# Optimization experiments

Measured on AMD Instinct MI355X. Metric: run time of the kernel, lower is better.

The kernel has to match this reference:

```python
import jax, jax.numpy as jnp
import numpy as np

WS = 8          # window size
HEADS = 16      # num heads

def conv2d(x, w, padding=0, groups=1):
    return jax.lax.conv_general_dilated(
        x, w, window_strides=(1, 1),
        padding=((padding, padding), (padding, padding)),
        feature_group_count=groups,
        dimension_numbers=('NCHW', 'OIHW', 'NCHW'))

def bn(x, scale, bias):  # inference BN folded into per-channel affine
    return x * scale[None, :, None, None] + bias[None, :, None, None]

def relative_position_index(ws):
    coords = np.stack(np.meshgrid(np.arange(ws), np.arange(ws), indexing='ij'))  # (2, ws, ws)
    cf = coords.reshape(2, -1)
    rc = (cf[:, :, None] - cf[:, None, :]).transpose(1, 2, 0)  # (n, n, 2)
    rc[:, :, 0] += ws - 1
    rc[:, :, 1] += ws - 1
    rc[:, :, 0] *= 2 * ws - 1
    return rc.sum(-1)  # (n, n) int

def avg_pool(x, kh, kw, ph, pw):
    # AvgPool2d with count_include_pad=True (zero pad, divide by full kernel size)
    s = jax.lax.reduce_window(x, 0.0, jax.lax.add, (1, 1, kh, kw), (1, 1, 1, 1),
                              ((0, 0), (0, 0), (ph, ph), (pw, pw)))
    return s / (kh * kw)

def setup_inputs() -> dict:
    key = jax.random.key(0)
    ks = jax.random.split(key, 12)
    C = 256
    x = jax.random.normal(ks[0], (4, C, 128, 128), dtype=jnp.float32)
    inp = {
        'x': x,
        'qkv_w':     jax.random.normal(ks[1], (3 * C, C, 1, 1), jnp.float32) * 0.05,
        'local1_w':  jax.random.normal(ks[2], (C, C, 3, 3), jnp.float32) * 0.05,
        'local1_scale': jnp.ones((C,), jnp.float32),
        'local1_bias':  jnp.zeros((C,), jnp.float32),
        'local2_w':  jax.random.normal(ks[3], (C, C, 1, 1), jnp.float32) * 0.05,
        'local2_scale': jnp.ones((C,), jnp.float32),
        'local2_bias':  jnp.zeros((C,), jnp.float32),
        'dw_w':      jax.random.normal(ks[4], (C, 1, WS, WS), jnp.float32) * 0.05,
        'proj_scale': jnp.ones((C,), jnp.float32),
        'proj_bias':  jnp.zeros((C,), jnp.float32),
        'pw_w':      jax.random.normal(ks[5], (C, C, 1, 1), jnp.float32) * 0.05,
        'rel_bias_table': jax.random.normal(ks[6], ((2 * WS - 1) ** 2, HEADS), jnp.float32) * 0.02,
    }
    return inp

def reference(x, qkv_w, local1_w, local1_scale, local1_bias,
              local2_w, local2_scale, local2_bias,
              dw_w, proj_scale, proj_bias, pw_w, rel_bias_table):
    B, C, H, W = x.shape
    ws, h = WS, HEADS
    d = C // h
    scale = d ** -0.5

    # local branches
    local = bn(conv2d(x, local2_w, padding=0), local2_scale, local2_bias) \
          + bn(conv2d(x, local1_w, padding=1), local1_scale, local1_bias)

    # reflect-pad to multiple of ws (static shapes)
    pad_h = (ws - H % ws) % ws
    pad_w = (ws - W % ws) % ws
    xp = x
    if pad_w:
        xp = jnp.pad(xp, ((0, 0), (0, 0), (0, 0), (0, pad_w)), mode='reflect')
    if pad_h:
        xp = jnp.pad(xp, ((0, 0), (0, 0), (0, pad_h), (0, 0)), mode='reflect')
    Hp, Wp = xp.shape[2], xp.shape[3]
    hh, ww = Hp // ws, Wp // ws

    # qkv: 1x1 conv, then window partition
    qkv = conv2d(xp, qkv_w)  # (B, 3C, Hp, Wp)
    qkv = qkv.reshape(B, 3, h, d, hh, ws, ww, ws)
    qkv = qkv.transpose(1, 0, 4, 6, 2, 5, 7, 3)  # (3, B, hh, ww, h, ws, ws, d)
    qkv = qkv.reshape(3, B * hh * ww, h, ws * ws, d)
    q, k, v = qkv[0], qkv[1], qkv[2]

    dots = jnp.einsum('whid,whjd->whij', q, k) * scale
    rpi = relative_position_index(ws)  # (n, n)
    bias = rel_bias_table[rpi.reshape(-1)].reshape(ws * ws, ws * ws, h)
    dots = dots + bias.transpose(2, 0, 1)[None]
    attn = jax.nn.softmax(dots, axis=-1)
    out = jnp.einsum('whij,whjd->whid', attn, v)

    # windows back to image
    out = out.reshape(B, hh, ww, h, ws, ws, d)
    out = out.transpose(0, 3, 6, 1, 4, 2, 5).reshape(B, C, Hp, Wp)
    out = out[:, :, :H, :W]

    # boundary smoothing avg pools (reflect pad 1 then zero-padded avg pool)
    ax = avg_pool(jnp.pad(out, ((0, 0), (0, 0), (0, 1), (0, 0)), mode='reflect'),
                  ws, 1, ws // 2 - 1, 0)
    ay = avg_pool(jnp.pad(out, ((0, 0), (0, 0), (0, 0), (0, 1)), mode='reflect'),
                  1, ws, 0, ws // 2 - 1)
    out = ax + ay + local

    # pad_out + separable conv projection
    out = jnp.pad(out, ((0, 0), (0, 0), (0, 1), (0, 1)), mode='reflect')
    out = conv2d(out, dw_w, padding=(ws - 1) // 2, groups=C)  # depthwise 8x8
    out = bn(out, proj_scale, proj_bias)
    out = conv2d(out, pw_w)  # pointwise 1x1
    return out[:, :, :H, :W]
```

## Files before the change

### kernel.cpp

```cpp
#include <hip/hip_runtime.h>
#include <cstddef>

#define HH 128
#define WW2 128
#define HWSZ (HH*WW2)
#define CCH 256

typedef __attribute__((ext_vector_type(8))) short short8v;
typedef __attribute__((ext_vector_type(16))) float f32x16;
typedef __attribute__((ext_vector_type(4)))  float f32x4;

__device__ __forceinline__ ushort bf16rte(float v) {
    uint u = __float_as_uint(v);
    uint r = u + 0x7FFFu + ((u >> 16) & 1u);
    return (ushort)(r >> 16);
}

__global__ __launch_bounds__(256) void k_fold(const float* __restrict__ l1w, const float* __restrict__ l1s,
                                              const float* __restrict__ l1b, const float* __restrict__ l2w,
                                              const float* __restrict__ l2s, const float* __restrict__ l2b,
                                              float* __restrict__ Wf, float* __restrict__ biasf) {
    int idx = blockIdx.x * 256 + threadIdx.x;
    if (idx < 2304 * 256) {
        int co = idx & 255;
        int i2 = idx >> 8;
        int ci = i2 / 9;
        int k  = i2 - ci * 9;
        float w = l1s[co] * l1w[co * 2304 + ci * 9 + k];
        if (k == 4) w += l2s[co] * l2w[co * 256 + ci];
        Wf[i2 * 256 + co] = w;
    }
    if (idx < 256) biasf[idx] = l1b[idx] + l2b[idx];
}

__global__ __launch_bounds__(256) void k_wsplit(const float* __restrict__ Wf,
                                                ushort* __restrict__ ahi, ushort* __restrict__ alo) {
    int idx = blockIdx.x * 256 + threadIdx.x;
    if (idx >= 589824) return;
    int j    = idx & 7;
    int lane = (idx >> 3) & 63;
    int t2   = idx >> 9;
    int kb   = t2 % 144;
    int cob  = t2 / 144;
    int cc  = kb / 18; int rem = kb - cc * 18; int tap = rem >> 1; int ks = rem & 1;
    int ci  = cc * 32 + ks * 16 + ((lane >> 5) << 3) + j;
    int co  = cob * 32 + (lane & 31);
    float v = Wf[(size_t)(ci * 9 + tap) * 256 + co];
    ushort h = bf16rte(v);
    float hf = __uint_as_float((uint)h << 16);
    ushort l = bf16rte(v - hf);
    ahi[idx] = h;
    alo[idx] = l;
}

__global__ __launch_bounds__(256) void k_aswz(const float* __restrict__ qkvw,
                                              ushort* __restrict__ aqh, ushort* __restrict__ aql) {
    int idx = blockIdx.x * 256 + threadIdx.x;
    if (idx >= 196608) return;
    int j    = idx & 7;
    int lane = (idx >> 3) & 63;
    int t2   = idx >> 9;
    int kk   = t2 & 7;
    int hp   = t2 >> 3;
    int p    = hp % 3, h = hp / 3;
    int co = p * 256 + h * 16 + (lane & 15);
    int ci = kk * 32 + ((lane >> 4) << 3) + j;
    float v = qkvw[(size_t)co * 256 + ci];
    ushort hi = bf16rte(v);
    float hf = __uint_as_float((uint)hi << 16);
    aqh[idx] = hi;
    aql[idx] = bf16rte(v - hf);
}

__global__ __launch_bounds__(256) void k_pswz(const float* __restrict__ pww,
                                              ushort* __restrict__ apwh, ushort* __restrict__ apwl) {
    int idx = blockIdx.x * 256 + threadIdx.x;
    if (idx >= 65536) return;
    int j    = idx & 7;
    int lane = (idx >> 3) & 63;
    int t2   = idx >> 9;
    int ks   = t2 & 15;
    int cob  = t2 >> 4;
    int co = cob * 32 + (lane & 31);
    int ci = ks * 16 + ((lane >> 5) << 3) + j;
    float v = pww[(size_t)co * 256 + ci];
    ushort h = bf16rte(v);
    float hf = __uint_as_float((uint)h << 16);
    apwh[idx] = h;
    apwl[idx] = bf16rte(v - hf);
}

__global__ __launch_bounds__(256) void k_cvt(const float* __restrict__ x,
                                             ushort* __restrict__ xhi, ushort* __restrict__ xlo) {
    __shared__ uint pk[32 * 265];
    int t = threadIdx.x;
    int bid = blockIdx.x;
    int b = bid >> 9;
    int px0 = (bid & 511) * 32;
    const float* xb = x + (size_t)b * CCH * HWSZ;
    for (int step = 0; step < 32; ++step) {
        int ci = step * 8 + (t >> 5);
        float v = xb[(size_t)ci * HWSZ + px0 + (t & 31)];
        ushort h = bf16rte(v);
        float hf = __uint_as_float((uint)h << 16);
        ushort l = bf16rte(v - hf);
        pk[(t & 31) * 265 + ci] = ((uint)h << 16) | l;
    }
    __syncthreads();
    int pxl = t >> 3, o = t & 7;
    uint* hp = (uint*)xhi;
    uint* lp = (uint*)xlo;
    size_t pb2 = ((size_t)b * HWSZ + px0 + pxl) * 128;
#pragma unroll
    for (int m = 0; m < 16; ++m) {
        int cip = m * 16 + o * 2;
        uint p0 = pk[pxl * 265 + cip];
        uint p1 = pk[pxl * 265 + cip + 1];
        hp[pb2 + m * 8 + o] = (p1 & 0xFFFF0000u) | (p0 >> 16);
        lp[pb2 + m * 8 + o] = (p1 << 16) | (p0 & 0xFFFFu);
    }
}

__global__ __launch_bounds__(256) void k_conv3m(const ushort* __restrict__ xhi, const ushort* __restrict__ xlo,
                                                const ushort* __restrict__ afr_hi, const ushort* __restrict__ afr_lo,
                                                const float* __restrict__ biasf, float* __restrict__ outp) {
    __shared__ __align__(16) ushort Xsh[12960];
    char* xsb = (char*)Xsh;

    int t = threadIdx.x;
    int bid = blockIdx.x;
    int cb = bid & 1;
    int t2 = bid >> 1;
    int tile_c = t2 & 7;
    int tile_r = (t2 >> 3) & 15;
    int b = t2 >> 7;
    int x0 = tile_c * 16, y0 = tile_r * 8;

    int w = t >> 6, lane = t & 63;
    int co_w = cb * 128 + (w >> 1) * 64;
    int pr0 = (w & 1) * 4;
    int pr_l = (lane & 31) >> 4;
    int pc = lane & 15;
    int kl = lane >> 5;
    int lb0 = (pr0 + 0 + pr_l) * 1296 + pc * 72 + kl * 16;
    int lb1 = (pr0 + 2 + pr_l) * 1296 + pc * 72 + kl * 16;

    const short8v* Ahi = (const short8v*)afr_hi;
    const short8v* Alo = (const short8v*)afr_lo;
    int cobase = (co_w >> 5) * 144 * 64;

    f32x16 c00 = {}, c01 = {}, c10 = {}, c11 = {};

    for (int cc = 0; cc < 8; ++cc) {
        __syncthreads();
#pragma unroll
        for (int it = 0; it < 6; ++it) {
            int i = t + it * 256;
            if (i < 1440) {
                int oct = i & 3;
                int j2 = i >> 2;
                int plane = j2 & 1;
                int loc = j2 >> 1;
                int r = loc / 18, c = loc - r * 18;
                int gy = y0 - 1 + r, gx = x0 - 1 + c;
                uint4 v = make_uint4(0u, 0u, 0u, 0u);
                if (gy >= 0 && gy < 128 && gx >= 0 && gx < 128) {
                    const ushort* src = plane ? xlo : xhi;
                    v = *(const uint4*)(src + ((size_t)(b * HWSZ + gy * 128 + gx) * 256 + cc * 32 + oct * 8));
                }
                *(uint4*)(xsb + plane * 12960 + loc * 72 + oct * 16) = v;
            }
        }
        __syncthreads();

        int baseA = cobase + cc * 18 * 64 + lane;
#pragma unroll
        for (int tap = 0; tap < 9; ++tap) {
            const int ky = tap / 3, kx = tap - ky * 3;
#pragma unroll
            for (int ks = 0; ks < 2; ++ks) {
                const int boff = ky * 1296 + kx * 72 + ks * 32;
                short8v b0h = *(const short8v*)(xsb + lb0 + boff);
                short8v b0l = *(const short8v*)(xsb + lb0 + boff + 12960);
                short8v b1h = *(const short8v*)(xsb + lb1 + boff);
                short8v b1l = *(const short8v*)(xsb + lb1 + boff + 12960);
                int ai = baseA + (tap * 2 + ks) * 64;
                short8v a0h = Ahi[ai];
                short8v a0l = Alo[ai];
                short8v a1h = Ahi[ai + 144 * 64];
                short8v a1l = Alo[ai + 144 * 64];
                c00 = __builtin_amdgcn_mfma_f32_32x32x16_bf16(a0h, b0h, c00, 0, 0, 0);
                c00 = __builtin_amdgcn_mfma_f32_32x32x16_bf16(a0h, b0l, c00, 0, 0, 0);
                c00 = __builtin_amdgcn_mfma_f32_32x32x16_bf16(a0l, b0h, c00, 0, 0, 0);
                c01 = __builtin_amdgcn_mfma_f32_32x32x16_bf16(a0h, b1h, c01, 0, 0, 0);
                c01 = __builtin_amdgcn_mfma_f32_32x32x16_bf16(a0h, b1l, c01, 0, 0, 0);
                c01 = __builtin_amdgcn_mfma_f32_32x32x16_bf16(a0l, b1h, c01, 0, 0, 0);
                c10 = __builtin_amdgcn_mfma_f32_32x32x16_bf16(a1h, b0h, c10, 0, 0, 0);
                c10 = __builtin_amdgcn_mfma_f32_32x32x16_bf16(a1h, b0l, c10, 0, 0, 0);
                c10 = __builtin_amdgcn_mfma_f32_32x32x16_bf16(a1l, b0h, c10, 0, 0, 0);
                c11 = __builtin_amdgcn_mfma_f32_32x32x16_bf16(a1h, b1h, c11, 0, 0, 0);
                c11 = __builtin_amdgcn_mfma_f32_32x32x16_bf16(a1h, b1l, c11, 0, 0, 0);
                c11 = __builtin_amdgcn_mfma_f32_32x32x16_bf16(a1l, b1h, c11, 0, 0, 0);
            }
        }
    }

    int colg = x0 + pc;
    int row0 = y0 + pr0 + pr_l;
    int row1 = row0 + 2;
#pragma unroll
    for (int r = 0; r < 16; ++r) {
        int rr = (r & 3) + 8 * (r >> 2) + 4 * kl;
        {
            int co = co_w + rr;
            float bv = biasf[co];
            float* ob = outp + ((size_t)(b * CCH + co)) * HWSZ;
            ob[row0 * 128 + colg] = c00[r] + bv;
            ob[row1 * 128 + colg] = c01[r] + bv;
        }
        {
            int co = co_w + 32 + rr;
            float bv = biasf[co];
            float* ob = outp + ((size_t)(b * CCH + co)) * HWSZ;
            ob[row0 * 128 + colg] = c10[r] + bv;
            ob[row1 * 128 + colg] = c11[r] + bv;
        }
    }
}

__global__ __launch_bounds__(256, 3) void k_attn(const ushort* __restrict__ xhi, const ushort* __restrict__ xlo,
                                                 const ushort* __restrict__ aqh, const ushort* __restrict__ aql,
                                                 const float* __restrict__ bt, float* __restrict__ attnout) {
    __shared__ float qkvb[2][48 * 64];
    __shared__ float btl[16 * 225];

    int t = threadIdx.x;
    int wv = __builtin_amdgcn_readfirstlane(t >> 6);
    int lane = t & 63;
    int widx = blockIdx.x;
    int b = widx >> 8;
    int rem = widx & 255;
    int hy = rem >> 4, wx = rem & 15;
    int y0 = hy * 8, x0 = wx * 8;

    for (int i = t; i < 3600; i += 256) {
        int rpi = i >> 4, hh = i & 15;
        btl[hh * 225 + rpi] = bt[i];
    }

    int tokb = (wv << 4) | (lane & 15);
    int pixb = (y0 + (tokb >> 3)) * 128 + (x0 + (tokb & 7));
    const ushort* xbh = xhi + ((size_t)b * HWSZ + pixb) * 256 + ((lane >> 4) << 3);
    const ushort* xbl = xlo + ((size_t)b * HWSZ + pixb) * 256 + ((lane >> 4) << 3);
    short8v bh_[8], bl_[8];
#pragma unroll
    for (int kk = 0; kk < 8; ++kk) {
        bh_[kk] = *(const short8v*)(xbh + kk * 32);
        bl_[kk] = *(const short8v*)(xbl + kk * 32);
    }

    const short8v* AhB = (const short8v*)aqh + lane;
    const short8v* AlB = (const short8v*)aql + lane;
    int wrow = ((lane >> 4) << 2);
    int wtok = (wv << 4) + (lane & 15);

    {
#pragma unroll
        for (int p = 0; p < 3; ++p) {
            f32x4 c = {};
#pragma unroll
            for (int kk = 0; kk < 8; ++kk) {
                short8v ah = AhB[(p * 8 + kk) * 64];
                short8v al = AlB[(p * 8 + kk) * 64];
                c = __builtin_amdgcn_mfma_f32_16x16x32_bf16(ah, bh_[kk], c, 0, 0, 0);
                c = __builtin_amdgcn_mfma_f32_16x16x32_bf16(ah, bl_[kk], c, 0, 0, 0);
                c = __builtin_amdgcn_mfma_f32_16x16x32_bf16(al, bh_[kk], c, 0, 0, 0);
            }
            float* bw = &qkvb[0][(p * 16 + wrow) * 64 + wtok];
            bw[0] = c[0]; bw[64] = c[1]; bw[128] = c[2]; bw[192] = c[3];
        }
    }
    __syncthreads();

    int irow = wv * 16 + (lane & 15);
    int jg = lane >> 4;
    int iy = irow >> 3, ix = irow & 7;

#pragma unroll 2
    for (int h = 0; h < 16; ++h) {
        int h2 = (h + 1) & 15;
        int nb = (h + 1) & 1;
        const short8v* Ah = AhB + (size_t)h2 * 24 * 64;
        const short8v* Al = AlB + (size_t)h2 * 24 * 64;
#pragma unroll
        for (int p = 0; p < 3; ++p) {
            f32x4 c = {};
#pragma unroll
            for (int kk = 0; kk < 8; ++kk) {
                short8v ah = Ah[(p * 8 + kk) * 64];
                short8v al = Al[(p * 8 + kk) * 64];
                c = __builtin_amdgcn_mfma_f32_16x16x32_bf16(ah, bh_[kk], c, 0, 0, 0);
                c = __builtin_amdgcn_mfma_f32_16x16x32_bf16(ah, bl_[kk], c, 0, 0, 0);
                c = __builtin_amdgcn_mfma_f32_16x16x32_bf16(al, bh_[kk], c, 0, 0, 0);
            }
            float* bw = &qkvb[nb][(p * 16 + wrow) * 64 + wtok];
            bw[0] = c[0]; bw[64] = c[1]; bw[128] = c[2]; bw[192] = c[3];
        }

        const float* buf = qkvb[h & 1];
        float qd[16];
#pragma unroll
        for (int d = 0; d < 16; ++d) qd[d] = buf[d * 64 + irow];
        float s[16];
#pragma unroll
        for (int jj = 0; jj < 16; ++jj) s[jj] = 0.f;
#pragma unroll
        for (int d = 0; d < 16; ++d) {
            const float* kp = &buf[(16 + d) * 64 + jg * 16];
#pragma unroll
            for (int m = 0; m < 4; ++m) {
                float4 kv = *(const float4*)(kp + m * 4);
                s[m * 4 + 0] += qd[d] * kv.x;
                s[m * 4 + 1] += qd[d] * kv.y;
                s[m * 4 + 2] += qd[d] * kv.z;
                s[m * 4 + 3] += qd[d] * kv.w;
            }
        }
#pragma unroll
        for (int jj = 0; jj < 16; ++jj) {
            int j = jg * 16 + jj;
            int jy = j >> 3, jx = j & 7;
            int rpi = (iy - jy + 7) * 15 + (ix - jx + 7);
            s[jj] = s[jj] * 0.25f + btl[h * 225 + rpi];
        }
        float mx = s[0];
#pragma unroll
        for (int jj = 1; jj < 16; ++jj) mx = fmaxf(mx, s[jj]);
        mx = fmaxf(mx, __shfl_xor(mx, 16));
        mx = fmaxf(mx, __shfl_xor(mx, 32));
        float ls = 0.f;
#pragma unroll
        for (int jj = 0; jj < 16; ++jj) { s[jj] = __expf(s[jj] - mx); ls += s[jj]; }
        ls += __shfl_xor(ls, 16);
        ls += __shfl_xor(ls, 32);
        float inv = 1.0f / ls;
#pragma unroll
        for (int d = 0; d < 16; ++d) {
            const float* vp = &buf[(32 + d) * 64 + jg * 16];
            float o0 = 0.f, o1 = 0.f;
#pragma unroll
            for (int m = 0; m < 4; ++m) {
                float4 vvv = *(const float4*)(vp + m * 4);
                o0 += s[m * 4 + 0] * vvv.x + s[m * 4 + 1] * vvv.y;
                o1 += s[m * 4 + 2] * vvv.z + s[m * 4 + 3] * vvv.w;
            }
            float o = o0 + o1;
            o += __shfl_xor(o, 16);
            o += __shfl_xor(o, 32);
            if (jg == 0)
                attnout[((size_t)(b * CCH + h * 16 + d)) * HWSZ + (y0 + iy) * 128 + (x0 + ix)] = o * inv;
        }
        __syncthreads();
    }
}

__global__ __launch_bounds__(256) void k_pools(const float* __restrict__ attnout, const float* __restrict__ localb,
                                               float* __restrict__ sbuf) {
    for (int i = blockIdx.x * 256 + threadIdx.x; i < 4 * CCH * HWSZ; i += gridDim.x * 256) {
        int xc = i & 127;
        int y  = (i >> 7) & 127;
        int bc = i >> 14;
        const float* pl = attnout + (size_t)bc * HWSZ;
        float axs = 0.f;
#pragma unroll
        for (int d = -3; d <= 4; ++d) {
            int t2 = y + d;
            if (t2 >= 0 && t2 < 128) axs += pl[t2 * 128 + xc];
        }
        if (y >= 124) axs += pl[126 * 128 + xc];
        float ays = 0.f;
#pragma unroll
        for (int d = -3; d <= 4; ++d) {
            int t2 = xc + d;
            if (t2 >= 0 && t2 < 128) ays += pl[y * 128 + t2];
        }
        if (xc >= 124) ays += pl[y * 128 + 126];
        sbuf[i] = (axs + ays) * 0.125f + localb[i];
    }
}

__device__ __forceinline__ void dw_loadrow(const float* __restrict__ sp, int trow, int j, float* dst) {
    if (trow < 0 || trow > 128) {
#pragma unroll
        for (int q = 0; q < 8; ++q) dst[q] = 0.f;
        return;
    }
    int sr = (trow == 128) ? 126 : trow;
    const float* rp = sp + sr * 128;
#pragma unroll
    for (int q = 0; q < 8; ++q) {
        int col = j - 3 + q;
        float v = 0.f;
        if (col >= 0 && col <= 128) v = rp[(col == 128) ? 126 : col];
        dst[q] = v;
    }
}

__global__ __launch_bounds__(256) void k_dw(const float* __restrict__ sbuf, const float* __restrict__ dww,
                                            const float* __restrict__ pscale, const float* __restrict__ pbias,
                                            float* __restrict__ tbuf) {
    int t = threadIdx.x;
    int j = t & 127;
    int half = __builtin_amdgcn_readfirstlane(t >> 7);
    int bid = blockIdx.x;
    int c = (bid & 127) * 2 + half;
    int b = bid >> 7;
    const float* sp = sbuf + ((size_t)(b * CCH + c)) * HWSZ;
    float wloc[64];
    const float* dwp = dww + c * 64;
#pragma unroll
    for (int i = 0; i < 64; ++i) wloc[i] = dwp[i];
    float scale = pscale[c], bias = pbias[c];

    float rbuf[8][8];
#pragma unroll
    for (int tr = -3; tr <= 4; ++tr) {
        dw_loadrow(sp, tr, j, rbuf[(tr + 8) & 7]);
    }
    float* op = tbuf + ((size_t)(b * CCH + c)) * HWSZ;
    for (int yb = 0; yb < 16; ++yb) {
#pragma unroll
        for (int k = 0; k < 8; ++k) {
            int y = yb * 8 + k;
            float a0 = 0.f, a1 = 0.f, a2 = 0.f, a3 = 0.f;
#pragma unroll
            for (int p = 0; p < 8; ++p) {
                const int slot = (k + 5 + p) & 7;
                float part = 0.f;
#pragma unroll
                for (int q = 0; q < 8; ++q) part += wloc[p * 8 + q] * rbuf[slot][q];
                if ((p & 3) == 0) a0 += part;
                else if ((p & 3) == 1) a1 += part;
                else if ((p & 3) == 2) a2 += part;
                else a3 += part;
            }
            op[y * 128 + j] = scale * ((a0 + a1) + (a2 + a3)) + bias;
            dw_loadrow(sp, y + 5, j, rbuf[(k + 5) & 7]);
        }
    }
}

__global__ __launch_bounds__(256) void k_pwm(const float* __restrict__ tbuf,
                                             const ushort* __restrict__ apwh, const ushort* __restrict__ apwl,
                                             float* __restrict__ outp) {
    __shared__ __align__(16) ushort pBh[32][264];
    __shared__ __align__(16) ushort pBl[32][264];

    int t = threadIdx.x;
    int bid = blockIdx.x;
    int b = bid >> 9;
    int px0 = (bid & 511) * 32;
    int px = t & 31;

    for (int it = 0; it < 32; ++it) {
        int ci = it * 8 + (t >> 5);
        float v = tbuf[((size_t)(b * CCH + ci)) * HWSZ + px0 + px];
        ushort h = bf16rte(v);
        float hf = __uint_as_float((uint)h << 16);
        pBh[px][ci] = h;
        pBl[px][ci] = bf16rte(v - hf);
    }
    __syncthreads();

    int w = t >> 6, lane = t & 63;
    int kl = lane >> 5;
    int pc = lane & 31;
    const short8v* Ah = (const short8v*)apwh;
    const short8v* Al = (const short8v*)apwl;
    int a0base = ((w * 2) * 16) * 64 + lane;
    int a1base = ((w * 2 + 1) * 16) * 64 + lane;

    f32x16 c0 = {}, c1 = {};
#pragma unroll
    for (int ks = 0; ks < 16; ++ks) {
        short8v bh = *(const short8v*)&pBh[pc][ks * 16 + kl * 8];
        short8v bl = *(const short8v*)&pBl[pc][ks * 16 + kl * 8];
        short8v a0h = Ah[a0base + ks * 64];
        short8v a0l = Al[a0base + ks * 64];
        short8v a1h = Ah[a1base + ks * 64];
        short8v a1l = Al[a1base + ks * 64];
        c0 = __builtin_amdgcn_mfma_f32_32x32x16_bf16(a0h, bh, c0, 0, 0, 0);
        c0 = __builtin_amdgcn_mfma_f32_32x32x16_bf16(a0h, bl, c0, 0, 0, 0);
        c0 = __builtin_amdgcn_mfma_f32_32x32x16_bf16(a0l, bh, c0, 0, 0, 0);
        c1 = __builtin_amdgcn_mfma_f32_32x32x16_bf16(a1h, bh, c1, 0, 0, 0);
        c1 = __builtin_amdgcn_mfma_f32_32x32x16_bf16(a1h, bl, c1, 0, 0, 0);
        c1 = __builtin_amdgcn_mfma_f32_32x32x16_bf16(a1l, bh, c1, 0, 0, 0);
    }

#pragma unroll
    for (int r = 0; r < 16; ++r) {
        int rr = (r & 3) + 8 * (r >> 2) + 4 * kl;
        {
            int co = w * 64 + rr;
            outp[((size_t)(b * CCH + co)) * HWSZ + px0 + pc] = c0[r];
        }
        {
            int co = w * 64 + 32 + rr;
            outp[((size_t)(b * CCH + co)) * HWSZ + px0 + pc] = c1[r];
        }
    }
}

extern "C" void kernel_launch(void* const* d_in, const int* in_sizes, int n_in,
                              void* d_out, int out_size, void* d_ws, size_t ws_size,
                              hipStream_t stream) {
    const float* x    = (const float*)d_in[0];
    const float* qkvw = (const float*)d_in[1];
    const float* l1w  = (const float*)d_in[2];
    const float* l1s  = (const float*)d_in[3];
    const float* l1b  = (const float*)d_in[4];
    const float* l2w  = (const float*)d_in[5];
    const float* l2s  = (const float*)d_in[6];
    const float* l2b  = (const float*)d_in[7];
    const float* dww  = (const float*)d_in[8];
    const float* ps   = (const float*)d_in[9];
    const float* pb   = (const float*)d_in[10];
    const float* pww  = (const float*)d_in[11];
    const float* bt   = (const float*)d_in[12];
    float* out = (float*)d_out;
    float* wsf = (float*)d_ws;

    const size_t nWf = 589824;
    const size_t nPlane = 16777216;
    const size_t nAq = 196608;
    const size_t nApw = 65536;
    size_t need = (nWf + 256 + 3 * nPlane) * sizeof(float)
                + (2 * 589824 + 2 * nAq + 2 * nApw) * sizeof(ushort);
    if (ws_size < need) return;

    float* Wf      = wsf;
    float* biasf   = wsf + nWf;
    float* attnout = wsf + nWf + 256;
    float* localb  = attnout + nPlane;
    float* sbuf    = localb + nPlane;
    float* tbuf    = attnout;
    ushort* xhi = (ushort*)sbuf;
    ushort* xlo = xhi + nPlane;
    ushort* ahi = (ushort*)(sbuf + nPlane);
    ushort* alo = ahi + 589824;
    ushort* aqh = alo + 589824;
    ushort* aql = aqh + nAq;
    ushort* apwh = aql + nAq;
    ushort* apwl = apwh + nApw;

    k_fold  <<<2304, 256, 0, stream>>>(l1w, l1s, l1b, l2w, l2s, l2b, Wf, biasf);
    k_wsplit<<<2304, 256, 0, stream>>>(Wf, ahi, alo);
    k_aswz  <<<768,  256, 0, stream>>>(qkvw, aqh, aql);
    k_pswz  <<<256,  256, 0, stream>>>(pww, apwh, apwl);
    k_cvt   <<<2048, 256, 0, stream>>>(x, xhi, xlo);
    k_conv3m<<<1024, 256, 0, stream>>>(xhi, xlo, ahi, alo, biasf, localb);
    k_attn  <<<1024, 256, 0, stream>>>(xhi, xlo, aqh, aql, bt, attnout);
    k_pools <<<4096, 256, 0, stream>>>(attnout, localb, sbuf);
    k_dw    <<<512,  256, 0, stream>>>(sbuf, dww, ps, pb, tbuf);
    k_pwm   <<<2048, 256, 0, stream>>>(tbuf, apwh, apwl, out);
}
```

Measured before the change: 796.5 us.

## Double-buffer conv3x3 input tile in LDS with register prefetch

The 3x3 conv kernel now keeps two LDS buffers for the input halo tile. It loads the next channel chunk from global memory into registers before running the MFMA loop on the current buffer, then writes those registers to the other buffer after a barrier. The aim is to hide global load latency behind the MFMA work and to drop one barrier per iteration. In exchange it doubles LDS use to about 52KB, which may lower occupancy, and adds 24 VGPRs for staging.

```diff
diff --git a/kernel.cpp b/kernel.cpp
--- a/kernel.cpp
+++ b/kernel.cpp
@@ -124,7 +124,7 @@
 __global__ __launch_bounds__(256) void k_conv3m(const ushort* __restrict__ xhi, const ushort* __restrict__ xlo,
                                                 const ushort* __restrict__ afr_hi, const ushort* __restrict__ afr_lo,
                                                 const float* __restrict__ biasf, float* __restrict__ outp) {
-    __shared__ __align__(16) ushort Xsh[12960];
+    __shared__ __align__(16) ushort Xsh[2 * 12960];
     char* xsb = (char*)Xsh;
 
     int t = threadIdx.x;
@@ -151,8 +151,28 @@
 
     f32x16 c00 = {}, c01 = {}, c10 = {}, c11 = {};
 
-    for (int cc = 0; cc < 8; ++cc) {
-        __syncthreads();
+    uint4 st[6];
+    auto stage_issue = [&](int cc) {
+#pragma unroll
+        for (int it = 0; it < 6; ++it) {
+            int i = t + it * 256;
+            uint4 v = make_uint4(0u, 0u, 0u, 0u);
+            if (i < 1440) {
+                int oct = i & 3;
+                int j2 = i >> 2;
+                int plane = j2 & 1;
+                int loc = j2 >> 1;
+                int r = loc / 18, c = loc - r * 18;
+                int gy = y0 - 1 + r, gx = x0 - 1 + c;
+                if (gy >= 0 && gy < 128 && gx >= 0 && gx < 128) {
+                    const ushort* src = plane ? xlo : xhi;
+                    v = *(const uint4*)(src + ((size_t)(b * HWSZ + gy * 128 + gx) * 256 + cc * 32 + oct * 8));
+                }
+            }
+            st[it] = v;
+        }
+    };
+    auto stage_write = [&](int buf) {
 #pragma unroll
         for (int it = 0; it < 6; ++it) {
             int i = t + it * 256;
@@ -161,17 +181,20 @@
                 int j2 = i >> 2;
                 int plane = j2 & 1;
                 int loc = j2 >> 1;
-                int r = loc / 18, c = loc - r * 18;
-                int gy = y0 - 1 + r, gx = x0 - 1 + c;
-                uint4 v = make_uint4(0u, 0u, 0u, 0u);
-                if (gy >= 0 && gy < 128 && gx >= 0 && gx < 128) {
-                    const ushort* src = plane ? xlo : xhi;
-                    v = *(const uint4*)(src + ((size_t)(b * HWSZ + gy * 128 + gx) * 256 + cc * 32 + oct * 8));
-                }
-                *(uint4*)(xsb + plane * 12960 + loc * 72 + oct * 16) = v;
-            }
-        }
-        __syncthreads();
+                *(uint4*)(xsb + buf * 25920 + plane * 12960 + loc * 72 + oct * 16) = st[it];
+            }
+        }
+    };
+
+    stage_issue(0);
+    asm volatile("s_waitcnt vmcnt(0)" ::: "memory");
+    stage_write(0);
+    asm volatile("s_waitcnt lgkmcnt(0)" ::: "memory");
+    __builtin_amdgcn_s_barrier();
+
+    for (int cc = 0; cc < 8; ++cc) {
+        if (cc < 7) stage_issue(cc + 1);
+        int bufoff = (cc & 1) * 25920;
 
         int baseA = cobase + cc * 18 * 64 + lane;
 #pragma unroll
@@ -179,7 +202,7 @@
             const int ky = tap / 3, kx = tap - ky * 3;
 #pragma unroll
             for (int ks = 0; ks < 2; ++ks) {
-                const int boff = ky * 1296 + kx * 72 + ks * 32;
+                const int boff = bufoff + ky * 1296 + kx * 72 + ks * 32;
                 short8v b0h = *(const short8v*)(xsb + lb0 + boff);
                 short8v b0l = *(const short8v*)(xsb + lb0 + boff + 12960);
                 short8v b1h = *(const short8v*)(xsb + lb1 + boff);
@@ -203,6 +226,13 @@
                 c11 = __builtin_amdgcn_mfma_f32_32x32x16_bf16(a1l, b1h, c11, 0, 0, 0);
             }
         }
+
+        if (cc < 7) {
+            asm volatile("s_waitcnt vmcnt(0)" ::: "memory");
+            stage_write((cc + 1) & 1);
+            asm volatile("s_waitcnt lgkmcnt(0)" ::: "memory");
+            __builtin_amdgcn_s_barrier();
+        }
     }
 
     int colg = x0 + pc;
```

After: 794.0 us. No clear change (-0.3%).

## Merge local 3x3 conv and window attention into one interleaved kernel

Applied to the files above, without the earlier changes.

Folds the conv3m and attention kernels into a single launch where even blocks run the 3x3 conv tile and odd blocks run a window's attention, sharing one LDS allocation. The aim is to run the MFMA-heavy conv alongside the more ALU/LDS-bound attention on the same CUs and to drop a launch boundary and its tail. In exchange, both block types now take the larger shared-memory footprint and the register budget of the heavier path. Attention also loses its launch_bounds occupancy hint, which may reduce its occupancy.

```diff
diff --git a/kernel.cpp b/kernel.cpp
--- a/kernel.cpp
+++ b/kernel.cpp
@@ -121,246 +121,245 @@
     }
 }
 
-__global__ __launch_bounds__(256) void k_conv3m(const ushort* __restrict__ xhi, const ushort* __restrict__ xlo,
-                                                const ushort* __restrict__ afr_hi, const ushort* __restrict__ afr_lo,
-                                                const float* __restrict__ biasf, float* __restrict__ outp) {
-    __shared__ __align__(16) ushort Xsh[12960];
-    char* xsb = (char*)Xsh;
-
+__global__ __launch_bounds__(256) void k_convattn(const ushort* __restrict__ xhi, const ushort* __restrict__ xlo,
+                                                  const ushort* __restrict__ afr_hi, const ushort* __restrict__ afr_lo,
+                                                  const ushort* __restrict__ aqh, const ushort* __restrict__ aql,
+                                                  const float* __restrict__ biasf, const float* __restrict__ bt,
+                                                  float* __restrict__ localb, float* __restrict__ attnout) {
+    __shared__ __align__(16) char smem[38976];
     int t = threadIdx.x;
-    int bid = blockIdx.x;
-    int cb = bid & 1;
-    int t2 = bid >> 1;
-    int tile_c = t2 & 7;
-    int tile_r = (t2 >> 3) & 15;
-    int b = t2 >> 7;
-    int x0 = tile_c * 16, y0 = tile_r * 8;
-
-    int w = t >> 6, lane = t & 63;
-    int co_w = cb * 128 + (w >> 1) * 64;
-    int pr0 = (w & 1) * 4;
-    int pr_l = (lane & 31) >> 4;
-    int pc = lane & 15;
-    int kl = lane >> 5;
-    int lb0 = (pr0 + 0 + pr_l) * 1296 + pc * 72 + kl * 16;
-    int lb1 = (pr0 + 2 + pr_l) * 1296 + pc * 72 + kl * 16;
-
-    const short8v* Ahi = (const short8v*)afr_hi;
-    const short8v* Alo = (const short8v*)afr_lo;
-    int cobase = (co_w >> 5) * 144 * 64;
-
-    f32x16 c00 = {}, c01 = {}, c10 = {}, c11 = {};
-
-    for (int cc = 0; cc < 8; ++cc) {
+
+    if ((blockIdx.x & 1) == 0) {
+        char* xsb = smem;
+        int bid = blockIdx.x >> 1;
+        int cb = bid & 1;
+        int t2 = bid >> 1;
+        int tile_c = t2 & 7;
+        int tile_r = (t2 >> 3) & 15;
+        int b = t2 >> 7;
+        int x0 = tile_c * 16, y0 = tile_r * 8;
+
+        int w = t >> 6, lane = t & 63;
+        int co_w = cb * 128 + (w >> 1) * 64;
+        int pr0 = (w & 1) * 4;
+        int pr_l = (lane & 31) >> 4;
+        int pc = lane & 15;
+        int kl = lane >> 5;
+        int lb0 = (pr0 + 0 + pr_l) * 1296 + pc * 72 + kl * 16;
+        int lb1 = (pr0 + 2 + pr_l) * 1296 + pc * 72 + kl * 16;
+
+        const short8v* Ahi = (const short8v*)afr_hi;
+        const short8v* Alo = (const short8v*)afr_lo;
+        int cobase = (co_w >> 5) * 144 * 64;
+
+        f32x16 c00 = {}, c01 = {}, c10 = {}, c11 = {};
+
+        for (int cc = 0; cc < 8; ++cc) {
+            __syncthreads();
+#pragma unroll
+            for (int it = 0; it < 6; ++it) {
+                int i = t + it * 256;
+                if (i < 1440) {
+                    int oct = i & 3;
+                    int j2 = i >> 2;
+                    int plane = j2 & 1;
+                    int loc = j2 >> 1;
+                    int r = loc / 18, c = loc - r * 18;
+                    int gy = y0 - 1 + r, gx = x0 - 1 + c;
+                    uint4 v = make_uint4(0u, 0u, 0u, 0u);
+                    if (gy >= 0 && gy < 128 && gx >= 0 && gx < 128) {
+                        const ushort* src = plane ? xlo : xhi;
+                        v = *(const uint4*)(src + ((size_t)(b * HWSZ + gy * 128 + gx) * 256 + cc * 32 + oct * 8));
+                    }
+                    *(uint4*)(xsb + plane * 12960 + loc * 72 + oct * 16) = v;
+                }
+            }
+            __syncthreads();
+
+            int baseA = cobase + cc * 18 * 64 + lane;
+#pragma unroll
+            for (int tap = 0; tap < 9; ++tap) {
+                const int ky = tap / 3, kx = tap - ky * 3;
+#pragma unroll
+                for (int ks = 0; ks < 2; ++ks) {
+                    const int boff = ky * 1296 + kx * 72 + ks * 32;
+                    short8v b0h = *(const short8v*)(xsb + lb0 + boff);
+                    short8v b0l = *(const short8v*)(xsb + lb0 + boff + 12960);
+                    short8v b1h = *(const short8v*)(xsb + lb1 + boff);
+                    short8v b1l = *(const short8v*)(xsb + lb1 + boff + 12960);
+                    int ai = baseA + (tap * 2 + ks) * 64;
+                    short8v a0h = Ahi[ai];
+                    short8v a0l = Alo[ai];
+                    short8v a1h = Ahi[ai + 144 * 64];
+                    short8v a1l = Alo[ai + 144 * 64];
+                    c00 = __builtin_amdgcn_mfma_f32_32x32x16_bf16(a0h, b0h, c00, 0, 0, 0);
+                    c00 = __builtin_amdgcn_mfma_f32_32x32x16_bf16(a0h, b0l, c00, 0, 0, 0);
+                    c00 = __builtin_amdgcn_mfma_f32_32x32x16_bf16(a0l, b0h, c00, 0, 0, 0);
+                    c01 = __builtin_amdgcn_mfma_f32_32x32x16_bf16(a0h, b1h, c01, 0, 0, 0);
+                    c01 = __builtin_amdgcn_mfma_f32_32x32x16_bf16(a0h, b1l, c01, 0, 0, 0);
+                    c01 = __builtin_amdgcn_mfma_f32_32x32x16_bf16(a0l, b1h, c01, 0, 0, 0);
+                    c10 = __builtin_amdgcn_mfma_f32_32x32x16_bf16(a1h, b0h, c10, 0, 0, 0);
+                    c10 = __builtin_amdgcn_mfma_f32_32x32x16_bf16(a1h, b0l, c10, 0, 0, 0);
+                    c10 = __builtin_amdgcn_mfma_f32_32x32x16_bf16(a1l, b0h, c10, 0, 0, 0);
+                    c11 = __builtin_amdgcn_mfma_f32_32x32x16_bf16(a1h, b1h, c11, 0, 0, 0);
+                    c11 = __builtin_amdgcn_mfma_f32_32x32x16_bf16(a1h, b1l, c11, 0, 0, 0);
+                    c11 = __builtin_amdgcn_mfma_f32_32x32x16_bf16(a1l, b1h, c11, 0, 0, 0);
+                }
+            }
+        }
+
+        int colg = x0 + pc;
+        int row0 = y0 + pr0 + pr_l;
+        int row1 = row0 + 2;
+#pragma unroll
+        for (int r = 0; r < 16; ++r) {
+            int rr = (r & 3) + 8 * (r >> 2) + 4 * kl;
+            {
+                int co = co_w + rr;
+                float bv = biasf[co];
+                float* ob = localb + ((size_t)(b * CCH + co)) * HWSZ;
+                ob[row0 * 128 + colg] = c00[r] + bv;
+                ob[row1 * 128 + colg] = c01[r] + bv;
+            }
+            {
+                int co = co_w + 32 + rr;
+                float bv = biasf[co];
+                float* ob = localb + ((size_t)(b * CCH + co)) * HWSZ;
+                ob[row0 * 128 + colg] = c10[r] + bv;
+                ob[row1 * 128 + colg] = c11[r] + bv;
+            }
+        }
+    } else {
+        float* qkvb = (float*)smem;
+        float* btl  = (float*)(smem + 24576);
+
+        int wv = __builtin_amdgcn_readfirstlane(t >> 6);
+        int lane = t & 63;
+        int widx = blockIdx.x >> 1;
+        int b = widx >> 8;
+        int rem = widx & 255;
+        int hy = rem >> 4, wx = rem & 15;
+        int y0 = hy * 8, x0 = wx * 8;
+
+        for (int i = t; i < 3600; i += 256) {
+            int rpi = i >> 4, hh = i & 15;
+            btl[hh * 225 + rpi] = bt[i];
+        }
+
+        int tokb = (wv << 4) | (lane & 15);
+        int pixb = (y0 + (tokb >> 3)) * 128 + (x0 + (tokb & 7));
+        const ushort* xbh = xhi + ((size_t)b * HWSZ + pixb) * 256 + ((lane >> 4) << 3);
+        const ushort* xbl = xlo + ((size_t)b * HWSZ + pixb) * 256 + ((lane >> 4) << 3);
+        short8v bh_[8], bl_[8];
+#pragma unroll
+        for (int kk = 0; kk < 8; ++kk) {
+            bh_[kk] = *(const short8v*)(xbh + kk * 32);
+            bl_[kk] = *(const short8v*)(xbl + kk * 32);
+        }
+
+        const short8v* AhB = (const short8v*)aqh + lane;
+        const short8v* AlB = (const short8v*)aql + lane;
+        int wrow = ((lane >> 4) << 2);
+        int wtok = (wv << 4) + (lane & 15);
+
+        {
+#pragma unroll
+            for (int p = 0; p < 3; ++p) {
+                f32x4 c = {};
+#pragma unroll
+                for (int kk = 0; kk < 8; ++kk) {
+                    short8v ah = AhB[(p * 8 + kk) * 64];
+                    short8v al = AlB[(p * 8 + kk) * 64];
+                    c = __builtin_amdgcn_mfma_f32_16x16x32_bf16(ah, bh_[kk], c, 0, 0, 0);
+                    c = __builtin_amdgcn_mfma_f32_16x16x32_bf16(ah, bl_[kk], c, 0, 0, 0);
+                    c = __builtin_amdgcn_mfma_f32_16x16x32_bf16(al, bh_[kk], c, 0, 0, 0);
+                }
+                float* bw = &qkvb[(p * 16 + wrow) * 64 + wtok];
+                bw[0] = c[0]; bw[64] = c[1]; bw[128] = c[2]; bw[192] = c[3];
+            }
+        }
         __syncthreads();
-#pragma unroll
-        for (int it = 0; it < 6; ++it) {
-            int i = t + it * 256;
-            if (i < 1440) {
-                int oct = i & 3;
-                int j2 = i >> 2;
-                int plane = j2 & 1;
-                int loc = j2 >> 1;
-                int r = loc / 18, c = loc - r * 18;
-                int gy = y0 - 1 + r, gx = x0 - 1 + c;
-                uint4 v = make_uint4(0u, 0u, 0u, 0u);
-                if (gy >= 0 && gy < 128 && gx >= 0 && gx < 128) {
-                    const ushort* src = plane ? xlo : xhi;
-                    v = *(const uint4*)(src + ((size_t)(b * HWSZ + gy * 128 + gx) * 256 + cc * 32 + oct * 8));
+
+        int irow = wv * 16 + (lane & 15);
+        int jg = lane >> 4;
+        int iy = irow >> 3, ix = irow & 7;
+
+#pragma unroll 2
+        for (int h = 0; h < 16; ++h) {
+            int h2 = (h + 1) & 15;
+            int nb = (h + 1) & 1;
+            const short8v* Ah = AhB + (size_t)h2 * 24 * 64;
+            const short8v* Al = AlB + (size_t)h2 * 24 * 64;
+#pragma unroll
+            for (int p = 0; p < 3; ++p) {
+                f32x4 c = {};
+#pragma unroll
+                for (int kk = 0; kk < 8; ++kk) {
+                    short8v ah = Ah[(p * 8 + kk) * 64];
+                    short8v al = Al[(p * 8 + kk) * 64];
+                    c = __builtin_amdgcn_mfma_f32_16x16x32_bf16(ah, bh_[kk], c, 0, 0, 0);
+                    c = __builtin_amdgcn_mfma_f32_16x16x32_bf16(ah, bl_[kk], c, 0, 0, 0);
+                    c = __builtin_amdgcn_mfma_f32_16x16x32_bf16(al, bh_[kk], c, 0, 0, 0);
                 }
-                *(uint4*)(xsb + plane * 12960 + loc * 72 + oct * 16) = v;
-            }
-        }
-        __syncthreads();
-
-        int baseA = cobase + cc * 18 * 64 + lane;
-#pragma unroll
-        for (int tap = 0; tap < 9; ++tap) {
-            const int ky = tap / 3, kx = tap - ky * 3;
-#pragma unroll
-            for (int ks = 0; ks < 2; ++ks) {
-                const int boff = ky * 1296 + kx * 72 + ks * 32;
-                short8v b0h = *(const short8v*)(xsb + lb0 + boff);
-                short8v b0l = *(const short8v*)(xsb + lb0 + boff + 12960);
-                short8v b1h = *(const short8v*)(xsb + lb1 + boff);
-                short8v b1l = *(const short8v*)(xsb + lb1 + boff + 12960);
-                int ai = baseA + (tap * 2 + ks) * 64;
-                short8v a0h = Ahi[ai];
-                short8v a0l = Alo[ai];
-                short8v a1h = Ahi[ai + 144 * 64];
-                short8v a1l = Alo[ai + 144 * 64];
-                c00 = __builtin_amdgcn_mfma_f32_32x32x16_bf16(a0h, b0h, c00, 0, 0, 0);
-                c00 = __builtin_amdgcn_mfma_f32_32x32x16_bf16(a0h, b0l, c00, 0, 0, 0);
-                c00 = __builtin_amdgcn_mfma_f32_32x32x16_bf16(a0l, b0h, c00, 0, 0, 0);
-                c01 = __builtin_amdgcn_mfma_f32_32x32x16_bf16(a0h, b1h, c01, 0, 0, 0);
-                c01 = __builtin_amdgcn_mfma_f32_32x32x16_bf16(a0h, b1l, c01, 0, 0, 0);
-                c01 = __builtin_amdgcn_mfma_f32_32x32x16_bf16(a0l, b1h, c01, 0, 0, 0);
-                c10 = __builtin_amdgcn_mfma_f32_32x32x16_bf16(a1h, b0h, c10, 0, 0, 0);
-                c10 = __builtin_amdgcn_mfma_f32_32x32x16_bf16(a1h, b0l, c10, 0, 0, 0);
-                c10 = __builtin_amdgcn_mfma_f32_32x32x16_bf16(a1l, b0h, c10, 0, 0, 0);
-                c11 = __builtin_amdgcn_mfma_f32_32x32x16_bf16(a1h, b1h, c11, 0, 0, 0);
-                c11 = __builtin_amdgcn_mfma_f32_32x32x16_bf16(a1h, b1l, c11, 0, 0, 0);
-                c11 = __builtin_amdgcn_mfma_f32_32x32x16_bf16(a1l, b1h, c11, 0, 0, 0);
-            }
-        }
-    }
-
-    int colg = x0 + pc;
-    int row0 = y0 + pr0 + pr_l;
-    int row1 = row0 + 2;
-#pragma unroll
-    for (int r = 0; r < 16; ++r) {
-        int rr = (r & 3) + 8 * (r >> 2) + 4 * kl;
-        {
-            int co = co_w + rr;
-            float bv = biasf[co];
-            float* ob = outp + ((size_t)(b * CCH + co)) * HWSZ;
-            ob[row0 * 128 + colg] = c00[r] + bv;
-            ob[row1 * 128 + colg] = c01[r] + bv;
-        }
-        {
-            int co = co_w + 32 + rr;
-            float bv = biasf[co];
-            float* ob = outp + ((size_t)(b * CCH + co)) * HWSZ;
-            ob[row0 * 128 + colg] = c10[r] + bv;
-            ob[row1 * 128 + colg] = c11[r] + bv;
-        }
-    }
-}
-
-__global__ __launch_bounds__(256, 3) void k_attn(const ushort* __restrict__ xhi, const ushort* __restrict__ xlo,
-                                                 const ushort* __restrict__ aqh, const ushort* __restrict__ aql,
-                                                 const float* __restrict__ bt, float* __restrict__ attnout) {
-    __shared__ float qkvb[2][48 * 64];
-    __shared__ float btl[16 * 225];
-
-    int t = threadIdx.x;
-    int wv = __builtin_amdgcn_readfirstlane(t >> 6);
-    int lane = t & 63;
-    int widx = blockIdx.x;
-    int b = widx >> 8;
-    int rem = widx & 255;
-    int hy = rem >> 4, wx = rem & 15;
-    int y0 = hy * 8, x0 = wx * 8;
-
-    for (int i = t; i < 3600; i += 256) {
-        int rpi = i >> 4, hh = i & 15;
-        btl[hh * 225 + rpi] = bt[i];
-    }
-
-    int tokb = (wv << 4) | (lane & 15);
-    int pixb = (y0 + (tokb >> 3)) * 128 + (x0 + (tokb & 7));
-    const ushort* xbh = xhi + ((size_t)b * HWSZ + pixb) * 256 + ((lane >> 4) << 3);
-    const ushort* xbl = xlo + ((size_t)b * HWSZ + pixb) * 256 + ((lane >> 4) << 3);
-    short8v bh_[8], bl_[8];
-#pragma unroll
-    for (int kk = 0; kk < 8; ++kk) {
-        bh_[kk] = *(const short8v*)(xbh + kk * 32);
-        bl_[kk] = *(const short8v*)(xbl + kk * 32);
-    }
-
-    const short8v* AhB = (const short8v*)aqh + lane;
-    const short8v* AlB = (const short8v*)aql + lane;
-    int wrow = ((lane >> 4) << 2);
-    int wtok = (wv << 4) + (lane & 15);
-
-    {
-#pragma unroll
-        for (int p = 0; p < 3; ++p) {
-            f32x4 c = {};
-#pragma unroll
-            for (int kk = 0; kk < 8; ++kk) {
-                short8v ah = AhB[(p * 8 + kk) * 64];
-                short8v al = AlB[(p * 8 + kk) * 64];
-                c = __builtin_amdgcn_mfma_f32_16x16x32_bf16(ah, bh_[kk], c, 0, 0, 0);
-                c = __builtin_amdgcn_mfma_f32_16x16x32_bf16(ah, bl_[kk], c, 0, 0, 0);
-                c = __builtin_amdgcn_mfma_f32_16x16x32_bf16(al, bh_[kk], c, 0, 0, 0);
-            }
-            float* bw = &qkvb[0][(p * 16 + wrow) * 64 + wtok];
-            bw[0] = c[0]; bw[64] = c[1]; bw[128] = c[2]; bw[192] = c[3];
-        }
-    }
-    __syncthreads();
-
-    int irow = wv * 16 + (lane & 15);
-    int jg = lane >> 4;
-    int iy = irow >> 3, ix = irow & 7;
-
-#pragma unroll 2
-    for (int h = 0; h < 16; ++h) {
-        int h2 = (h + 1) & 15;
-        int nb = (h + 1) & 1;
-        const short8v* Ah = AhB + (size_t)h2 * 24 * 64;
-        const short8v* Al = AlB + (size_t)h2 * 24 * 64;
-#pragma unroll
-        for (int p = 0; p < 3; ++p) {
-            f32x4 c = {};
-#pragma unroll
-            for (int kk = 0; kk < 8; ++kk) {
-                short8v ah = Ah[(p * 8 + kk) * 64];
-                short8v al = Al[(p * 8 + kk) * 64];
-                c = __builtin_amdgcn_mfma_f32_16x16x32_bf16(ah, bh_[kk], c, 0, 0, 0);
-                c = __builtin_amdgcn_mfma_f32_16x16x32_bf16(ah, bl_[kk], c, 0, 0, 0);
-                c = __builtin_amdgcn_mfma_f32_16x16x32_bf16(al, bh_[kk], c, 0, 0, 0);
-            }
-            float* bw = &qkvb[nb][(p * 16 + wrow) * 64 + wtok];
-            bw[0] = c[0]; bw[64] = c[1]; bw[128] = c[2]; bw[192] = c[3];
-        }
-
-        const float* buf = qkvb[h & 1];
-        float qd[16];
-#pragma unroll
-        for (int d = 0; d < 16; ++d) qd[d] = buf[d * 64 + irow];
-        float s[16];
-#pragma unroll
-        for (int jj = 0; jj < 16; ++jj) s[jj] = 0.f;
-#pragma unroll
-        for (int d = 0; d < 16; ++d) {
-            const float* kp = &buf[(16 + d) * 64 + jg * 16];
-#pragma unroll
-            for (int m = 0; m < 4; ++m) {
-                float4 kv = *(const float4*)(kp + m * 4);
-                s[m * 4 + 0] += qd[d] * kv.x;
-                s[m * 4 + 1] += qd[d] * kv.y;
-                s[m * 4 + 2] += qd[d] * kv.z;
-                s[m * 4 + 3] += qd[d] * kv.w;
-            }
-        }
-#pragma unroll
-        for (int jj = 0; jj < 16; ++jj) {
-            int j = jg * 16 + jj;
-            int jy = j >> 3, jx = j & 7;
-            int rpi = (iy - jy + 7) * 15 + (ix - jx + 7);
-            s[jj] = s[jj] * 0.25f + btl[h * 225 + rpi];
-        }
-        float mx = s[0];
-#pragma unroll
-        for (int jj = 1; jj < 16; ++jj) mx = fmaxf(mx, s[jj]);
-        mx = fmaxf(mx, __shfl_xor(mx, 16));
-        mx = fmaxf(mx, __shfl_xor(mx, 32));
-        float ls = 0.f;
-#pragma unroll
-        for (int jj = 0; jj < 16; ++jj) { s[jj] = __expf(s[jj] - mx); ls += s[jj]; }
-        ls += __shfl_xor(ls, 16);
-        ls += __shfl_xor(ls, 32);
-        float inv = 1.0f / ls;
-#pragma unroll
-        for (int d = 0; d < 16; ++d) {
-            const float* vp = &buf[(32 + d) * 64 + jg * 16];
-            float o0 = 0.f, o1 = 0.f;
-#pragma unroll
-            for (int m = 0; m < 4; ++m) {
-                float4 vvv = *(const float4*)(vp + m * 4);
-                o0 += s[m * 4 + 0] * vvv.x + s[m * 4 + 1] * vvv.y;
-                o1 += s[m * 4 + 2] * vvv.z + s[m * 4 + 3] * vvv.w;
-            }
-            float o = o0 + o1;
-            o += __shfl_xor(o, 16);
-            o += __shfl_xor(o, 32);
-            if (jg == 0)
-                attnout[((size_t)(b * CCH + h * 16 + d)) * HWSZ + (y0 + iy) * 128 + (x0 + ix)] = o * inv;
-        }
-        __syncthreads();
+                float* bw = &qkvb[nb * 3072 + (p * 16 + wrow) * 64 + wtok];
+                bw[0] = c[0]; bw[64] = c[1]; bw[128] = c[2]; bw[192] = c[3];
+            }
+
+            const float* buf = qkvb + (h & 1) * 3072;
+            float qd[16];
+#pragma unroll
+            for (int d = 0; d < 16; ++d) qd[d] = buf[d * 64 + irow];
+            float s[16];
+#pragma unroll
+            for (int jj = 0; jj < 16; ++jj) s[jj] = 0.f;
+#pragma unroll
+            for (int d = 0; d < 16; ++d) {
+                const float* kp = &buf[(16 + d) * 64 + jg * 16];
+#pragma unroll
+                for (int m = 0; m < 4; ++m) {
+                    float4 kv = *(const float4*)(kp + m * 4);
+                    s[m * 4 + 0] += qd[d] * kv.x;
+                    s[m * 4 + 1] += qd[d] * kv.y;
+                    s[m * 4 + 2] += qd[d] * kv.z;
+                    s[m * 4 + 3] += qd[d] * kv.w;
+                }
+            }
+#pragma unroll
+            for (int jj = 0; jj < 16; ++jj) {
+                int j = jg * 16 + jj;
+                int jy = j >> 3, jx = j & 7;
+                int rpi = (iy - jy + 7) * 15 + (ix - jx + 7);
+                s[jj] = s[jj] * 0.25f + btl[h * 225 + rpi];
+            }
+            float mx = s[0];
+#pragma unroll
+            for (int jj = 1; jj < 16; ++jj) mx = fmaxf(mx, s[jj]);
+            mx = fmaxf(mx, __shfl_xor(mx, 16));
+            mx = fmaxf(mx, __shfl_xor(mx, 32));
+            float ls = 0.f;
+#pragma unroll
+            for (int jj = 0; jj < 16; ++jj) { s[jj] = __expf(s[jj] - mx); ls += s[jj]; }
+            ls += __shfl_xor(ls, 16);
+            ls += __shfl_xor(ls, 32);
+            float inv = 1.0f / ls;
+#pragma unroll
+            for (int d = 0; d < 16; ++d) {
+                const float* vp = &buf[(32 + d) * 64 + jg * 16];
+                float o0 = 0.f, o1 = 0.f;
+#pragma unroll
+                for (int m = 0; m < 4; ++m) {
+                    float4 vvv = *(const float4*)(vp + m * 4);
+                    o0 += s[m * 4 + 0] * vvv.x + s[m * 4 + 1] * vvv.y;
+                    o1 += s[m * 4 + 2] * vvv.z + s[m * 4 + 3] * vvv.w;
+                }
+                float o = o0 + o1;
+                o += __shfl_xor(o, 16);
+                o += __shfl_xor(o, 32);
+                if (jg == 0)
+                    attnout[((size_t)(b * CCH + h * 16 + d)) * HWSZ + (y0 + iy) * 128 + (x0 + ix)] = o * inv;
+            }
+            __syncthreads();
+        }
     }
 }
 
@@ -553,14 +552,13 @@
     ushort* apwh = aql + nAq;
     ushort* apwl = apwh + nApw;
 
-    k_fold  <<<2304, 256, 0, stream>>>(l1w, l1s, l1b, l2w, l2s, l2b, Wf, biasf);
-    k_wsplit<<<2304, 256, 0, stream>>>(Wf, ahi, alo);
-    k_aswz  <<<768,  256, 0, stream>>>(qkvw, aqh, aql);
-    k_pswz  <<<256,  256, 0, stream>>>(pww, apwh, apwl);
-    k_cvt   <<<2048, 256, 0, stream>>>(x, xhi, xlo);
-    k_conv3m<<<1024, 256, 0, stream>>>(xhi, xlo, ahi, alo, biasf, localb);
-    k_attn  <<<1024, 256, 0, stream>>>(xhi, xlo, aqh, aql, bt, attnout);
-    k_pools <<<4096, 256, 0, stream>>>(attnout, localb, sbuf);
-    k_dw    <<<512,  256, 0, stream>>>(sbuf, dww, ps, pb, tbuf);
-    k_pwm   <<<2048, 256, 0, stream>>>(tbuf, apwh, apwl, out);
-}
+    k_fold    <<<2304, 256, 0, stream>>>(l1w, l1s, l1b, l2w, l2s, l2b, Wf, biasf);
+    k_wsplit  <<<2304, 256, 0, stream>>>(Wf, ahi, alo);
+    k_aswz    <<<768,  256, 0, stream>>>(qkvw, aqh, aql);
+    k_pswz    <<<256,  256, 0, stream>>>(pww, apwh, apwl);
+    k_cvt     <<<2048, 256, 0, stream>>>(x, xhi, xlo);
+    k_convattn<<<2048, 256, 0, stream>>>(xhi, xlo, ahi, alo, aqh, aql, biasf, bt, localb, attnout);
+    k_pools   <<<4096, 256, 0, stream>>>(attnout, localb, sbuf);
+    k_dw      <<<512,  256, 0, stream>>>(sbuf, dww, ps, pb, tbuf);
+    k_pwm     <<<2048, 256, 0, stream>>>(tbuf, apwh, apwl, out);
+}
```

New measurement: 988.2 us. +24.1%, slower.

## Fuse boundary pooling and depthwise conv into one kernel via LDS plane

Applied to the files above, without the earlier changes.

Merges the avg-pool smoothing kernel and the 8x8 depthwise conv kernel into one kernel, with one block per (batch, channel) plane. Each block computes the pooled-plus-local plane into a 64 KB shared-memory buffer, then runs the depthwise conv out of LDS, with the two thread halves taking the top and bottom 64 rows. This removes the full-size intermediate buffer write and read to global memory and one kernel launch. In exchange, the large LDS footprint limits how many blocks fit on a CU, and the conv's row loads now come from LDS, where bank conflicts are possible.

```diff
diff --git a/kernel.cpp b/kernel.cpp
--- a/kernel.cpp
+++ b/kernel.cpp
@@ -364,32 +364,7 @@
     }
 }
 
-__global__ __launch_bounds__(256) void k_pools(const float* __restrict__ attnout, const float* __restrict__ localb,
-                                               float* __restrict__ sbuf) {
-    for (int i = blockIdx.x * 256 + threadIdx.x; i < 4 * CCH * HWSZ; i += gridDim.x * 256) {
-        int xc = i & 127;
-        int y  = (i >> 7) & 127;
-        int bc = i >> 14;
-        const float* pl = attnout + (size_t)bc * HWSZ;
-        float axs = 0.f;
-#pragma unroll
-        for (int d = -3; d <= 4; ++d) {
-            int t2 = y + d;
-            if (t2 >= 0 && t2 < 128) axs += pl[t2 * 128 + xc];
-        }
-        if (y >= 124) axs += pl[126 * 128 + xc];
-        float ays = 0.f;
-#pragma unroll
-        for (int d = -3; d <= 4; ++d) {
-            int t2 = xc + d;
-            if (t2 >= 0 && t2 < 128) ays += pl[y * 128 + t2];
-        }
-        if (xc >= 124) ays += pl[y * 128 + 126];
-        sbuf[i] = (axs + ays) * 0.125f + localb[i];
-    }
-}
-
-__device__ __forceinline__ void dw_loadrow(const float* __restrict__ sp, int trow, int j, float* dst) {
+__device__ __forceinline__ void dw_loadrow_lds(const float* sp, int trow, int j, float* dst) {
     if (trow < 0 || trow > 128) {
 #pragma unroll
         for (int q = 0; q < 8; ++q) dst[q] = 0.f;
@@ -406,16 +381,43 @@
     }
 }
 
-__global__ __launch_bounds__(256) void k_dw(const float* __restrict__ sbuf, const float* __restrict__ dww,
-                                            const float* __restrict__ pscale, const float* __restrict__ pbias,
-                                            float* __restrict__ tbuf) {
+__global__ __launch_bounds__(256) void k_pooldw(const float* __restrict__ attnout, const float* __restrict__ localb,
+                                                const float* __restrict__ dww,
+                                                const float* __restrict__ pscale, const float* __restrict__ pbias,
+                                                float* __restrict__ tbuf) {
+    __shared__ float spl[128 * 128];
     int t = threadIdx.x;
+    int bid = blockIdx.x;
+    int c = bid & 255;
+    int b = bid >> 8;
+    size_t plane = ((size_t)(b * CCH + c)) * HWSZ;
+    const float* pl = attnout + plane;
+    const float* lo = localb + plane;
+
+    for (int i = t; i < 16384; i += 256) {
+        int xc = i & 127;
+        int y  = i >> 7;
+        float axs = 0.f;
+#pragma unroll
+        for (int d = -3; d <= 4; ++d) {
+            int t2 = y + d;
+            if (t2 >= 0 && t2 < 128) axs += pl[t2 * 128 + xc];
+        }
+        if (y >= 124) axs += pl[126 * 128 + xc];
+        float ays = 0.f;
+#pragma unroll
+        for (int d = -3; d <= 4; ++d) {
+            int t2 = xc + d;
+            if (t2 >= 0 && t2 < 128) ays += pl[y * 128 + t2];
+        }
+        if (xc >= 124) ays += pl[y * 128 + 126];
+        spl[i] = (axs + ays) * 0.125f + lo[i];
+    }
+    __syncthreads();
+
     int j = t & 127;
-    int half = __builtin_amdgcn_readfirstlane(t >> 7);
-    int bid = blockIdx.x;
-    int c = (bid & 127) * 2 + half;
-    int b = bid >> 7;
-    const float* sp = sbuf + ((size_t)(b * CCH + c)) * HWSZ;
+    int yhalf = t >> 7;
+    int ybase = yhalf * 64;
     float wloc[64];
     const float* dwp = dww + c * 64;
 #pragma unroll
@@ -425,13 +427,13 @@
     float rbuf[8][8];
 #pragma unroll
     for (int tr = -3; tr <= 4; ++tr) {
-        dw_loadrow(sp, tr, j, rbuf[(tr + 8) & 7]);
-    }
-    float* op = tbuf + ((size_t)(b * CCH + c)) * HWSZ;
-    for (int yb = 0; yb < 16; ++yb) {
+        dw_loadrow_lds(spl, ybase + tr, j, rbuf[(tr + 8) & 7]);
+    }
+    float* op = tbuf + plane;
+    for (int yb = 0; yb < 8; ++yb) {
 #pragma unroll
         for (int k = 0; k < 8; ++k) {
-            int y = yb * 8 + k;
+            int y = ybase + yb * 8 + k;
             float a0 = 0.f, a1 = 0.f, a2 = 0.f, a3 = 0.f;
 #pragma unroll
             for (int p = 0; p < 8; ++p) {
@@ -445,7 +447,7 @@
                 else a3 += part;
             }
             op[y * 128 + j] = scale * ((a0 + a1) + (a2 + a3)) + bias;
-            dw_loadrow(sp, y + 5, j, rbuf[(k + 5) & 7]);
+            dw_loadrow_lds(spl, y + 5, j, rbuf[(k + 5) & 7]);
         }
     }
 }
@@ -560,7 +562,6 @@
     k_cvt   <<<2048, 256, 0, stream>>>(x, xhi, xlo);
     k_conv3m<<<1024, 256, 0, stream>>>(xhi, xlo, ahi, alo, biasf, localb);
     k_attn  <<<1024, 256, 0, stream>>>(xhi, xlo, aqh, aql, bt, attnout);
-    k_pools <<<4096, 256, 0, stream>>>(attnout, localb, sbuf);
-    k_dw    <<<512,  256, 0, stream>>>(sbuf, dww, ps, pb, tbuf);
+    k_pooldw<<<1024, 256, 0, stream>>>(attnout, localb, dww, ps, pb, tbuf);
     k_pwm   <<<2048, 256, 0, stream>>>(tbuf, apwh, apwl, out);
 }
```

Result: slower. 954.8 us (+19.9%).
